# Performance work log

Measured on AMD Instinct MI355X. Metric: run time of the kernel, lower is better.

## Reference

```python
import math
import jax, jax.numpy as jnp
import numpy as np

B, S, D, H = 2, 2048, 2048, 16
HD = D // H  # head_dim = 128, rotary_dim = HD (full rotation)
ROPE_BASE = 10000.0


def setup_inputs() -> dict:
    key = jax.random.key(0)
    k0, k1, k2 = jax.random.split(key, 3)
    return {
        "x": jax.random.normal(k0, (B, S, D), dtype=jnp.float32),
        "Wqkv": jax.random.normal(k1, (D, 3 * D), dtype=jnp.float32) * 0.02,
        "bqkv": jnp.zeros((3 * D,), dtype=jnp.float32),
        "Wout": jax.random.normal(k2, (D, D), dtype=jnp.float32) * 0.02,
        "bout": jnp.zeros((D,), dtype=jnp.float32),
    }


def _rope_cos_sin(seqlen, dim):
    # flash-attn RotaryEmbedding: inv_freq over even indices, outer with positions
    inv_freq = 1.0 / (ROPE_BASE ** (jnp.arange(0, dim, 2, dtype=jnp.float32) / dim))
    t = jnp.arange(seqlen, dtype=jnp.float32)
    freqs = jnp.outer(t, inv_freq)  # (S, dim/2)
    return jnp.cos(freqs), jnp.sin(freqs)


def reference(x, Wqkv, bqkv, Wout, bout):
    b, s, d = x.shape
    hd = d // H
    # fused QKV projection -> (B, S, 3, H, HD)
    qkv = (x @ Wqkv + bqkv).reshape(b, s, 3, H, hd)
    q, k, v = qkv[:, :, 0], qkv[:, :, 1], qkv[:, :, 2]  # (B,S,H,HD)

    cos, sin = _rope_cos_sin(s, hd)
    c = cos[:, None, :]  # (S,1,HD/2) broadcast over heads
    si = sin[:, None, :]

    def rot(t):
        # split-half rotary (as in apply_rotary_emb_qkv), computed in fp32
        t1, t2 = jnp.split(t.astype(jnp.float32), 2, axis=-1)
        return jnp.concatenate([t1 * c - t2 * si, t1 * si + t2 * c], axis=-1).astype(x.dtype)

    q = rot(q)
    k = rot(k)

    scale = 1.0 / math.sqrt(hd)
    scores = jnp.einsum("bthd,bshd->bhts", q, k * scale)  # (B,H,S,S)
    causal_mask = jnp.triu(jnp.full((s, s), -10000.0, dtype=scores.dtype), 1)
    attn = jax.nn.softmax(scores + causal_mask, axis=-1)
    ctx = jnp.einsum("bhts,bshd->bthd", attn, v).reshape(b, s, d)
    return ctx @ Wout + bout
```

## Files before the change

### kernel.cpp

```cpp
#include <hip/hip_runtime.h>
#include <hip/hip_bf16.h>

typedef __attribute__((ext_vector_type(4))) float fx4;
typedef __attribute__((ext_vector_type(8))) short bx8;
typedef __hip_bfloat16 bf16;

#define GLD16(dst, src)                                                        \
  __builtin_amdgcn_global_load_lds(                                            \
      (__attribute__((address_space(1))) void*)(src),                          \
      (__attribute__((address_space(3))) void*)(dst), 16, 0, 0)

__device__ inline float bf2f(short s_) {
  unsigned int u = ((unsigned int)(unsigned short)s_) << 16;
  float f;
  __builtin_memcpy(&f, &u, 4);
  return f;
}
__device__ inline short f2bf(float f) {
  __hip_bfloat16 h = __float2bfloat16(f);
  short r;
  __builtin_memcpy(&r, &h, 2);
  return r;
}

__global__ __launch_bounds__(256) void k_cast(const float* __restrict__ in,
                                              bf16* __restrict__ out, int n4) {
  int i = blockIdx.x * 256 + threadIdx.x;
  if (i >= n4) return;
  float4 v = reinterpret_cast<const float4*>(in)[i];
  bf16 t[4] = {__float2bfloat16(v.x), __float2bfloat16(v.y),
               __float2bfloat16(v.z), __float2bfloat16(v.w)};
  reinterpret_cast<ushort4*>(out)[i] = *reinterpret_cast<ushort4*>(t);
}

__global__ void k_tcast(const float* __restrict__ in, bf16* __restrict__ out,
                        int R, int C) {
  __shared__ float tile[32][33];
  int c0 = blockIdx.x * 32, r0 = blockIdx.y * 32;
  int tx = threadIdx.x, ty = threadIdx.y;
#pragma unroll
  for (int j = 0; j < 4; ++j)
    tile[ty + j * 8][tx] = in[(size_t)(r0 + ty + j * 8) * C + c0 + tx];
  __syncthreads();
#pragma unroll
  for (int j = 0; j < 4; ++j)
    out[(size_t)(c0 + ty + j * 8) * R + r0 + tx] =
        __float2bfloat16(tile[tx][ty + j * 8]);
}

__global__ __launch_bounds__(256) void k_ropetab(float* __restrict__ cosT,
                                                 float* __restrict__ sinT) {
  int idx = blockIdx.x * 256 + threadIdx.x;
  int t = idx >> 6, i = idx & 63;
  float inv = expf(-logf(10000.0f) * (float)i * (1.0f / 64.0f));
  float fr = (float)t * inv;
  cosT[idx] = cosf(fr);
  sinT[idx] = sinf(fr);
}

__global__ __launch_bounds__(256) void k_rope(bf16* __restrict__ qkv,
                                              const float* __restrict__ cosT,
                                              const float* __restrict__ sinT) {
  int t = blockIdx.x * 256 + threadIdx.x;
  int d0 = (t & 7) * 8;
  int qk = (t >> 3) & 1;
  int h = (t >> 4) & 15;
  int s = (t >> 8) & 2047;
  int b = (t >> 19) & 1;
  bf16* base = qkv + (size_t)(b * 2048 + s) * 6144 + qk * 2048 + h * 128;
  bx8 lo = *(const bx8*)(base + d0);
  bx8 hi = *(const bx8*)(base + 64 + d0);
  float4 ca = *(const float4*)&cosT[s * 64 + d0];
  float4 cb = *(const float4*)&cosT[s * 64 + d0 + 4];
  float4 sa = *(const float4*)&sinT[s * 64 + d0];
  float4 sb = *(const float4*)&sinT[s * 64 + d0 + 4];
  float c[8] = {ca.x, ca.y, ca.z, ca.w, cb.x, cb.y, cb.z, cb.w};
  float si[8] = {sa.x, sa.y, sa.z, sa.w, sb.x, sb.y, sb.z, sb.w};
  bx8 olo, ohi;
#pragma unroll
  for (int e = 0; e < 8; ++e) {
    float t1 = bf2f(lo[e]), t2 = bf2f(hi[e]);
    olo[e] = f2bf(t1 * c[e] - t2 * si[e]);
    ohi[e] = f2bf(t1 * si[e] + t2 * c[e]);
  }
  *(bx8*)(base + d0) = olo;
  *(bx8*)(base + 64 + d0) = ohi;
}

__global__ void k_vtrans(const bf16* __restrict__ qkv, bf16* __restrict__ vT) {
  __shared__ bf16 tile[32][33];
  int s0 = blockIdx.x * 32, d0 = blockIdx.y * 32, bh = blockIdx.z;
  int b = bh >> 4, h = bh & 15;
  int tx = threadIdx.x, ty = threadIdx.y;
#pragma unroll
  for (int j = 0; j < 4; ++j)
    tile[ty + j * 8][tx] =
        qkv[(size_t)(b * 2048 + s0 + ty + j * 8) * 6144 + 4096 + h * 128 + d0 + tx];
  __syncthreads();
#pragma unroll
  for (int j = 0; j < 4; ++j)
    vT[(size_t)(bh * 128 + d0 + ty + j * 8) * 2048 + s0 + tx] = tile[tx][ty + j * 8];
}

__global__ __launch_bounds__(512, 2) void k_gemm256(
    const bf16* __restrict__ A, const bf16* __restrict__ BT,
    const float* __restrict__ bias, bf16* __restrict__ C, int M, int N, int K,
    int NBX) {
  __shared__ __align__(16) bf16 As[2][2][256 * 32];
  __shared__ __align__(16) bf16 Bs[2][2][256 * 32];
  const int tid = threadIdx.x;
  const int lane = tid & 63, wid = tid >> 6;
  const int lr = lane & 15, lg = lane >> 4;
  const int wr = wid >> 2, wc = wid & 3;
  const int nwg = gridDim.x, bid = blockIdx.x;
  const int swz = (bid & 7) * (nwg >> 3) + (bid >> 3);
  const int mb = swz / NBX, nb = swz - mb * NBX;
  const int m0 = mb * 256, n0 = nb * 256;
  const int NT = K >> 6;

  fx4 acc[8][4];
#pragma unroll
  for (int m = 0; m < 8; ++m)
#pragma unroll
    for (int n = 0; n < 4; ++n) acc[m][n] = (fx4)(0.0f);

  auto SA = [&](int buf, int ks, int t) {
#pragma unroll
    for (int q = 0; q < 2; ++q) {
      const int L = q * 512 + tid;
      const int row = L >> 2, u = L & 3;
      GLD16(&As[buf][ks][L * 8],
            A + (size_t)(m0 + row) * K + t * 64 + ks * 32 + ((u ^ (row & 3)) * 8));
    }
  };
  auto SB = [&](int buf, int ks, int t) {
#pragma unroll
    for (int q = 0; q < 2; ++q) {
      const int L = q * 512 + tid;
      const int row = L >> 2, u = L & 3;
      GLD16(&Bs[buf][ks][L * 8],
            BT + (size_t)(n0 + row) * K + t * 64 + ks * 32 + ((u ^ (row & 3)) * 8));
    }
  };

  bx8 af[4], bfr[4];
  auto LDA = [&](int buf, int ks, int mh) {
#pragma unroll
    for (int m = 0; m < 4; ++m) {
      const int r = wr * 128 + mh * 64 + m * 16 + lr;
      af[m] = *(const bx8*)&As[buf][ks][r * 32 + ((lg ^ (r & 3)) * 8)];
    }
  };
  auto LDB = [&](int buf, int ks) {
#pragma unroll
    for (int n = 0; n < 4; ++n) {
      const int r = wc * 64 + n * 16 + lr;
      bfr[n] = *(const bx8*)&Bs[buf][ks][r * 32 + ((lg ^ (r & 3)) * 8)];
    }
  };

#define MFMA16(MH)                                                             \
  asm volatile("s_waitcnt lgkmcnt(0)" ::: "memory");                           \
  __builtin_amdgcn_sched_barrier(0);                                           \
  __builtin_amdgcn_s_setprio(1);                                               \
  _Pragma("unroll") for (int m = 0; m < 4; ++m)                                \
      _Pragma("unroll") for (int n = 0; n < 4; ++n) acc[(MH)*4 + m][n] =       \
          __builtin_amdgcn_mfma_f32_16x16x32_bf16(af[m], bfr[n],               \
                                                  acc[(MH)*4 + m][n], 0, 0, 0);\
  __builtin_amdgcn_s_setprio(0);                                               \
  __builtin_amdgcn_s_barrier();

  SA(0, 0, 0); SB(0, 0, 0);
  SA(0, 1, 0); SB(0, 1, 0);
  SA(1, 0, 1); SB(1, 0, 1);
  asm volatile("s_waitcnt vmcnt(8)" ::: "memory");
  __builtin_amdgcn_s_barrier();

  for (int t = 0; t < NT; ++t) {
    const int buf = t & 1;
    LDA(buf, 0, 0); LDB(buf, 0);
    if (t + 1 < NT) SA(buf ^ 1, 1, t + 1);
    __builtin_amdgcn_s_barrier();
    MFMA16(0)
    LDA(buf, 0, 1);
    if (t + 1 < NT) SB(buf ^ 1, 1, t + 1);
    asm volatile("s_waitcnt vmcnt(8)" ::: "memory");
    __builtin_amdgcn_s_barrier();
    MFMA16(1)
    LDA(buf, 1, 0); LDB(buf, 1);
    if (t + 2 < NT) SA(buf, 0, t + 2);
    __builtin_amdgcn_s_barrier();
    MFMA16(0)
    LDA(buf, 1, 1);
    if (t + 2 < NT) SB(buf, 0, t + 2);
    asm volatile("s_waitcnt vmcnt(8)" ::: "memory");
    __builtin_amdgcn_s_barrier();
    MFMA16(1)
  }
#undef MFMA16

  float bv[4];
#pragma unroll
  for (int n = 0; n < 4; ++n) bv[n] = bias[n0 + wc * 64 + n * 16 + lr];
#pragma unroll
  for (int mm = 0; mm < 8; ++mm)
#pragma unroll
    for (int n = 0; n < 4; ++n) {
      const int col = n0 + wc * 64 + n * 16 + lr;
#pragma unroll
      for (int j = 0; j < 4; ++j) {
        const int row = m0 + wr * 128 + mm * 16 + lg * 4 + j;
        C[(size_t)row * N + col] = __float2bfloat16(acc[mm][n][j] + bv[n]);
      }
    }
}

__global__ __launch_bounds__(256) void k_gemm_bt(
    const bf16* __restrict__ A, const bf16* __restrict__ BT,
    const float* __restrict__ bias, void* __restrict__ Cp, int M, int N, int K,
    int out_bf16) {
  __shared__ __align__(16) bf16 As[128 * 64];
  __shared__ __align__(16) bf16 Bs[128 * 64];
  const int tid = threadIdx.x;
  const int m0 = blockIdx.y * 128, n0 = blockIdx.x * 128;
  const int lane = tid & 63, w = tid >> 6;
  const int lr = lane & 15, lg = lane >> 4;
  const int wr = w >> 1, wc = w & 1;

  fx4 acc[4][4];
#pragma unroll
  for (int m = 0; m < 4; ++m)
#pragma unroll
    for (int n = 0; n < 4; ++n) acc[m][n] = (fx4)(0.0f);

  for (int kt = 0; kt < K; kt += 64) {
#pragma unroll
    for (int q = 0; q < 4; ++q) {
      const int slot = q * 256 + tid;
      const int row = slot >> 3, u = slot & 7;
      const int us = (u ^ (row & 7)) * 8;
      GLD16(&As[slot * 8], A + (size_t)(m0 + row) * K + kt + us);
      GLD16(&Bs[slot * 8], BT + (size_t)(n0 + row) * K + kt + us);
    }
    __syncthreads();
#pragma unroll
    for (int ks = 0; ks < 2; ++ks) {
      bx8 af[4], bf[4];
#pragma unroll
      for (int m = 0; m < 4; ++m) {
        const int r = wr * 64 + m * 16 + lr;
        const int u = ((ks * 4 + lg) ^ (lr & 7)) * 8;
        af[m] = *(const bx8*)&As[r * 64 + u];
      }
#pragma unroll
      for (int n = 0; n < 4; ++n) {
        const int r = wc * 64 + n * 16 + lr;
        const int u = ((ks * 4 + lg) ^ (lr & 7)) * 8;
        bf[n] = *(const bx8*)&Bs[r * 64 + u];
      }
#pragma unroll
      for (int m = 0; m < 4; ++m)
#pragma unroll
        for (int n = 0; n < 4; ++n)
          acc[m][n] =
              __builtin_amdgcn_mfma_f32_16x16x32_bf16(af[m], bf[n], acc[m][n], 0, 0, 0);
    }
    __syncthreads();
  }

  float bv[4];
#pragma unroll
  for (int n = 0; n < 4; ++n) bv[n] = bias[n0 + wc * 64 + n * 16 + lr];

#pragma unroll
  for (int m = 0; m < 4; ++m)
#pragma unroll
    for (int n = 0; n < 4; ++n) {
      const int col = n0 + wc * 64 + n * 16 + lr;
#pragma unroll
      for (int j = 0; j < 4; ++j) {
        const int row = m0 + wr * 64 + m * 16 + lg * 4 + j;
        const float v = acc[m][n][j] + bv[n];
        if (out_bf16)
          ((bf16*)Cp)[(size_t)row * N + col] = __float2bfloat16(v);
        else
          ((float*)Cp)[(size_t)row * N + col] = v;
      }
    }
}

__global__ __launch_bounds__(256) void k_zero(float4* __restrict__ p) {
  p[blockIdx.x * 256 + threadIdx.x] = make_float4(0.f, 0.f, 0.f, 0.f);
}

#define ATT_SL2E 0.12751740f

__global__ __launch_bounds__(256, 2) void k_attn2(
    const bf16* __restrict__ qkv, const bf16* __restrict__ vT,
    bf16* __restrict__ ctx, float* __restrict__ Of32, float* __restrict__ lf32) {
  __shared__ __align__(16) bf16 Ks[2][128 * 128];
  __shared__ __align__(16) bf16 Ps[4][32 * 64];
  const int tid = threadIdx.x;
  const int lane = tid & 63, w = tid >> 6;
  const int lr = lane & 15, lg = lane >> 4;
  const int bid = blockIdx.x;
  const int u = bid >> 5, bh = bid & 31;
  const int b = bh >> 4, h = bh & 15;
  int qt, t0, t1;
  if (u < 8) {
    qt = 8 + u; t0 = 0; t1 = 8;
  } else if (u < 16) {
    qt = 23 - u; t0 = 8; t1 = qt + 1;
  } else {
    qt = 23 - u; t0 = 0; t1 = qt + 1;
  }
  const int single = (u >= 16);
  const int nt = t1 - t0;

  const bf16* kbase = qkv + (size_t)b * 2048 * 6144 + 2048 + h * 128;
  const bf16* vbase = vT + (size_t)(b * 16 + h) * 128 * 2048;

  auto STAGE = [&](int bufi, int kt) {
    const int kv0 = kt * 128;
#pragma unroll
    for (int q = 0; q < 8; ++q) {
      const int slot = q * 256 + tid;
      const int row = slot >> 4, uu = slot & 15;
      GLD16(&Ks[bufi][slot * 8],
            kbase + (size_t)(kv0 + row) * 6144 + ((uu ^ (row & 15)) * 8));
    }
  };

  const bf16* qbase =
      qkv + (size_t)(b * 2048 + qt * 128 + w * 32) * 6144 + h * 128;
  bx8 qf[2][4];
#pragma unroll
  for (int m = 0; m < 2; ++m)
#pragma unroll
    for (int ks = 0; ks < 4; ++ks)
      qf[m][ks] = *(const bx8*)(qbase + (size_t)(m * 16 + lr) * 6144 + ks * 32 + lg * 8);

  bx8 vones;
#pragma unroll
  for (int e = 0; e < 8; ++e) vones[e] = (short)0x3F80;

  fx4 oacc[2][8], lacc[2];
#pragma unroll
  for (int m = 0; m < 2; ++m) {
    lacc[m] = (fx4)(0.0f);
#pragma unroll
    for (int d = 0; d < 8; ++d) oacc[m][d] = (fx4)(0.0f);
  }

  const int qrow0 = qt * 128 + w * 32;

  STAGE(0, t0);
  for (int i = 0; i < nt; ++i) {
    const int kt = t0 + i;
    const int cur = i & 1;
    if (i + 1 < nt) {
      STAGE(cur ^ 1, kt + 1);
      asm volatile("s_waitcnt vmcnt(8)" ::: "memory");
    } else {
      asm volatile("s_waitcnt vmcnt(0)" ::: "memory");
    }
    __builtin_amdgcn_s_barrier();
    asm volatile("" ::: "memory");

#pragma unroll
    for (int h2 = 0; h2 < 2; ++h2) {
      const int kv0 = kt * 128 + h2 * 64;
      if (kv0 > qrow0 + 31) continue;

      fx4 sacc[2][4];
#pragma unroll
      for (int n = 0; n < 4; ++n) {
        sacc[0][n] = (fx4)(0.0f);
        sacc[1][n] = (fx4)(0.0f);
      }
      __builtin_amdgcn_s_setprio(1);
#pragma unroll
      for (int n = 0; n < 4; ++n) {
        const int r = h2 * 64 + n * 16 + lr;
#pragma unroll
        for (int ks = 0; ks < 4; ++ks) {
          const bx8 kf = *(const bx8*)&Ks[cur][r * 128 + (((ks * 4 + lg) ^ lr) * 8)];
          sacc[0][n] =
              __builtin_amdgcn_mfma_f32_16x16x32_bf16(qf[0][ks], kf, sacc[0][n], 0, 0, 0);
          sacc[1][n] =
              __builtin_amdgcn_mfma_f32_16x16x32_bf16(qf[1][ks], kf, sacc[1][n], 0, 0, 0);
        }
      }
      __builtin_amdgcn_s_setprio(0);

      const bool needmask = (kv0 + 63) > qrow0;
#pragma unroll
      for (int n = 0; n < 4; ++n) {
        const int kvi = kv0 + n * 16 + lr;
#pragma unroll
        for (int m = 0; m < 2; ++m)
#pragma unroll
          for (int j = 0; j < 4; ++j) {
            float v = sacc[m][n][j] * ATT_SL2E;
            if (needmask) {
              const int qi = qrow0 + m * 16 + lg * 4 + j;
              if (kvi > qi) v = -200.0f;
            }
            const float p = exp2f(fminf(v, 60.0f));
            const int r = m * 16 + lg * 4 + j, c = n * 16 + lr;
            const int c2 = (c & 7) | (((c >> 3) ^ (r & 7)) << 3);
            Ps[w][r * 64 + c2] = __float2bfloat16(p);
          }
      }

      __builtin_amdgcn_s_setprio(1);
#pragma unroll
      for (int ks2 = 0; ks2 < 2; ++ks2) {
        const int uu = ((ks2 * 4 + lg) ^ (lr & 7)) * 8;
        const bx8 pf0 = *(const bx8*)&Ps[w][(0 * 16 + lr) * 64 + uu];
        const bx8 pf1 = *(const bx8*)&Ps[w][(1 * 16 + lr) * 64 + uu];
        lacc[0] = __builtin_amdgcn_mfma_f32_16x16x32_bf16(pf0, vones, lacc[0], 0, 0, 0);
        lacc[1] = __builtin_amdgcn_mfma_f32_16x16x32_bf16(pf1, vones, lacc[1], 0, 0, 0);
#pragma unroll
        for (int dn = 0; dn < 8; ++dn) {
          const bx8 vf = *(const bx8*)(vbase + (size_t)(dn * 16 + lr) * 2048 + kv0 +
                                       ks2 * 32 + lg * 8);
          oacc[0][dn] =
              __builtin_amdgcn_mfma_f32_16x16x32_bf16(pf0, vf, oacc[0][dn], 0, 0, 0);
          oacc[1][dn] =
              __builtin_amdgcn_mfma_f32_16x16x32_bf16(pf1, vf, oacc[1][dn], 0, 0, 0);
        }
      }
      __builtin_amdgcn_s_setprio(0);
    }
    __builtin_amdgcn_s_barrier();
    asm volatile("" ::: "memory");
  }

  if (single) {
    float rl[2][4];
#pragma unroll
    for (int m = 0; m < 2; ++m)
#pragma unroll
      for (int j = 0; j < 4; ++j) rl[m][j] = 1.0f / lacc[m][j];
#pragma unroll
    for (int m = 0; m < 2; ++m)
#pragma unroll
      for (int dn = 0; dn < 8; ++dn)
#pragma unroll
        for (int j = 0; j < 4; ++j) {
          const int row = qt * 128 + w * 32 + m * 16 + lg * 4 + j;
          ctx[(size_t)(b * 2048 + row) * 2048 + h * 128 + dn * 16 + lr] =
              __float2bfloat16(oacc[m][dn][j] * rl[m][j]);
        }
  } else {
    float* obase =
        Of32 + (((size_t)(b * 16 + h)) * 1024 + (qt * 128 - 1024 + w * 32)) * 128;
#pragma unroll
    for (int m = 0; m < 2; ++m)
#pragma unroll
      for (int dn = 0; dn < 8; ++dn)
#pragma unroll
        for (int j = 0; j < 4; ++j)
          atomicAdd(&obase[(m * 16 + lg * 4 + j) * 128 + dn * 16 + lr],
                    oacc[m][dn][j]);
    if (lr == 0) {
      float* lbase =
          lf32 + ((size_t)(b * 16 + h)) * 1024 + (qt * 128 - 1024 + w * 32);
#pragma unroll
      for (int m = 0; m < 2; ++m)
#pragma unroll
        for (int j = 0; j < 4; ++j)
          atomicAdd(&lbase[m * 16 + lg * 4 + j], lacc[m][j]);
    }
  }
}

__global__ __launch_bounds__(256) void k_norm(const float* __restrict__ Of32,
                                              const float* __restrict__ lf32,
                                              bf16* __restrict__ ctx) {
  const int idx = blockIdx.x * 256 + threadIdx.x;
  const size_t base = (size_t)idx * 8;
  const int d = base & 127;
  const size_t rowi = base >> 7;
  const float rl = 1.0f / lf32[rowi];
  const float4 a = *(const float4*)&Of32[base];
  const float4 c = *(const float4*)&Of32[base + 4];
  const int s = (int)(rowi & 1023);
  const int bh = (int)(rowi >> 10);
  const int b = bh >> 4, h = bh & 15;
  bf16 o[8] = {__float2bfloat16(a.x * rl), __float2bfloat16(a.y * rl),
               __float2bfloat16(a.z * rl), __float2bfloat16(a.w * rl),
               __float2bfloat16(c.x * rl), __float2bfloat16(c.y * rl),
               __float2bfloat16(c.z * rl), __float2bfloat16(c.w * rl)};
  *(ushort4*)&ctx[(size_t)(b * 2048 + 1024 + s) * 2048 + h * 128 + d] =
      *(ushort4*)o;
  *(ushort4*)&ctx[(size_t)(b * 2048 + 1024 + s) * 2048 + h * 128 + d + 4] =
      *(ushort4*)(o + 4);
}

extern "C" void kernel_launch(void* const* d_in, const int* in_sizes, int n_in,
                              void* d_out, int out_size, void* d_ws, size_t ws_size,
                              hipStream_t stream) {
  const float* x = (const float*)d_in[0];
  const float* Wqkv = (const float*)d_in[1];
  const float* bqkv = (const float*)d_in[2];
  const float* Wout = (const float*)d_in[3];
  const float* bout = (const float*)d_in[4];
  float* out = (float*)d_out;

  char* ws = (char*)d_ws;
  bf16* xb    = (bf16*)(ws + 0);
  bf16* wqkvT = (bf16*)(ws + 16777216);
  bf16* woutT = (bf16*)(ws + 41943040);
  bf16* qkvb  = (bf16*)(ws + 50331648);
  bf16* vTb   = (bf16*)(ws + 100663296);
  bf16* ctxb  = (bf16*)(ws + 117440512);
  float* cosT = (float*)(ws + 134217728);
  float* sinT = (float*)(ws + 134742016);
  float* Of32 = (float*)(ws + 135266304);
  float* lf32 = (float*)(ws + 152043520);

  k_zero<<<4128, 256, 0, stream>>>((float4*)Of32);
  k_cast<<<8192, 256, 0, stream>>>(x, xb, 2097152);
  k_tcast<<<dim3(192, 64), dim3(32, 8), 0, stream>>>(Wqkv, wqkvT, 2048, 6144);
  k_tcast<<<dim3(64, 64), dim3(32, 8), 0, stream>>>(Wout, woutT, 2048, 2048);
  k_ropetab<<<512, 256, 0, stream>>>(cosT, sinT);
  k_gemm256<<<384, 512, 0, stream>>>(xb, wqkvT, bqkv, qkvb, 4096, 6144, 2048, 24);
  k_rope<<<4096, 256, 0, stream>>>(qkvb, cosT, sinT);
  k_vtrans<<<dim3(64, 4, 32), dim3(32, 8), 0, stream>>>(qkvb, vTb);
  k_attn2<<<768, 256, 0, stream>>>(qkvb, vTb, ctxb, Of32, lf32);
  k_norm<<<2048, 256, 0, stream>>>(Of32, lf32, ctxb);
  k_gemm_bt<<<dim3(16, 32), 256, 0, stream>>>(ctxb, woutT, bout, out, 4096, 2048,
                                              2048, 0);
}
```

Measured before the change: 345.6 us.

## Shrink QKV GEMM tile to 256x128 and replace split-K atomics with two partial buffers

The QKV projection GEMM moves from a 256x256 tile with a two-substep K=64 pipeline to a 256x128 tile with a simple double-buffered K=32 loop. This doubles the grid to 768 blocks and raises the occupancy hint, at the cost of less operand reuse and a full vmcnt(0) wait every iteration. Separately, the split attention tiles now write plain stores into two partial O/l buffers instead of atomically adding into one zeroed buffer. The combine kernel sums the two partials and normalises them, and the zeroing kernel is removed. The partial buffers reuse workspace that held the already-consumed bf16 x and Wqkv^T.

```diff
diff --git a/kernel.cpp b/kernel.cpp
--- a/kernel.cpp
+++ b/kernel.cpp
@@ -102,115 +102,88 @@
     vT[(size_t)(bh * 128 + d0 + ty + j * 8) * 2048 + s0 + tx] = tile[tx][ty + j * 8];
 }
 
-__global__ __launch_bounds__(512, 2) void k_gemm256(
+__global__ __launch_bounds__(512, 4) void k_gemm256(
     const bf16* __restrict__ A, const bf16* __restrict__ BT,
     const float* __restrict__ bias, bf16* __restrict__ C, int M, int N, int K,
     int NBX) {
-  __shared__ __align__(16) bf16 As[2][2][256 * 32];
-  __shared__ __align__(16) bf16 Bs[2][2][256 * 32];
+  __shared__ __align__(16) bf16 As[2][256 * 32];
+  __shared__ __align__(16) bf16 Bs[2][128 * 32];
   const int tid = threadIdx.x;
   const int lane = tid & 63, wid = tid >> 6;
   const int lr = lane & 15, lg = lane >> 4;
-  const int wr = wid >> 2, wc = wid & 3;
+  const int wr = wid >> 1, wc = wid & 1;
   const int nwg = gridDim.x, bid = blockIdx.x;
   const int swz = (bid & 7) * (nwg >> 3) + (bid >> 3);
   const int mb = swz / NBX, nb = swz - mb * NBX;
-  const int m0 = mb * 256, n0 = nb * 256;
-  const int NT = K >> 6;
-
-  fx4 acc[8][4];
-#pragma unroll
-  for (int m = 0; m < 8; ++m)
+  const int m0 = mb * 256, n0 = nb * 128;
+  const int NT = K >> 5;
+
+  fx4 acc[4][4];
+#pragma unroll
+  for (int m = 0; m < 4; ++m)
 #pragma unroll
     for (int n = 0; n < 4; ++n) acc[m][n] = (fx4)(0.0f);
 
-  auto SA = [&](int buf, int ks, int t) {
+  auto SA = [&](int buf, int t) {
 #pragma unroll
     for (int q = 0; q < 2; ++q) {
       const int L = q * 512 + tid;
       const int row = L >> 2, u = L & 3;
-      GLD16(&As[buf][ks][L * 8],
-            A + (size_t)(m0 + row) * K + t * 64 + ks * 32 + ((u ^ (row & 3)) * 8));
+      GLD16(&As[buf][L * 8],
+            A + (size_t)(m0 + row) * K + t * 32 + ((u ^ ((row >> 1) & 3)) * 8));
     }
   };
-  auto SB = [&](int buf, int ks, int t) {
-#pragma unroll
-    for (int q = 0; q < 2; ++q) {
-      const int L = q * 512 + tid;
-      const int row = L >> 2, u = L & 3;
-      GLD16(&Bs[buf][ks][L * 8],
-            BT + (size_t)(n0 + row) * K + t * 64 + ks * 32 + ((u ^ (row & 3)) * 8));
-    }
+  auto SB = [&](int buf, int t) {
+    const int L = tid;
+    const int row = L >> 2, u = L & 3;
+    GLD16(&Bs[buf][L * 8],
+          BT + (size_t)(n0 + row) * K + t * 32 + ((u ^ ((row >> 1) & 3)) * 8));
   };
 
-  bx8 af[4], bfr[4];
-  auto LDA = [&](int buf, int ks, int mh) {
+  SA(0, 0); SB(0, 0);
+  asm volatile("s_waitcnt vmcnt(0)" ::: "memory");
+  __builtin_amdgcn_s_barrier();
+
+  for (int t = 0; t < NT; ++t) {
+    const int buf = t & 1;
+    if (t + 1 < NT) { SA(buf ^ 1, t + 1); SB(buf ^ 1, t + 1); }
+    bx8 af[4], bfr[4];
 #pragma unroll
     for (int m = 0; m < 4; ++m) {
-      const int r = wr * 128 + mh * 64 + m * 16 + lr;
-      af[m] = *(const bx8*)&As[buf][ks][r * 32 + ((lg ^ (r & 3)) * 8)];
-    }
-  };
-  auto LDB = [&](int buf, int ks) {
+      const int r = wr * 64 + m * 16 + lr;
+      af[m] = *(const bx8*)&As[buf][r * 32 + ((lg ^ ((r >> 1) & 3)) * 8)];
+    }
 #pragma unroll
     for (int n = 0; n < 4; ++n) {
       const int r = wc * 64 + n * 16 + lr;
-      bfr[n] = *(const bx8*)&Bs[buf][ks][r * 32 + ((lg ^ (r & 3)) * 8)];
-    }
-  };
-
-#define MFMA16(MH)                                                             \
-  asm volatile("s_waitcnt lgkmcnt(0)" ::: "memory");                           \
-  __builtin_amdgcn_sched_barrier(0);                                           \
-  __builtin_amdgcn_s_setprio(1);                                               \
-  _Pragma("unroll") for (int m = 0; m < 4; ++m)                                \
-      _Pragma("unroll") for (int n = 0; n < 4; ++n) acc[(MH)*4 + m][n] =       \
-          __builtin_amdgcn_mfma_f32_16x16x32_bf16(af[m], bfr[n],               \
-                                                  acc[(MH)*4 + m][n], 0, 0, 0);\
-  __builtin_amdgcn_s_setprio(0);                                               \
-  __builtin_amdgcn_s_barrier();
-
-  SA(0, 0, 0); SB(0, 0, 0);
-  SA(0, 1, 0); SB(0, 1, 0);
-  SA(1, 0, 1); SB(1, 0, 1);
-  asm volatile("s_waitcnt vmcnt(8)" ::: "memory");
-  __builtin_amdgcn_s_barrier();
-
-  for (int t = 0; t < NT; ++t) {
-    const int buf = t & 1;
-    LDA(buf, 0, 0); LDB(buf, 0);
-    if (t + 1 < NT) SA(buf ^ 1, 1, t + 1);
+      bfr[n] = *(const bx8*)&Bs[buf][r * 32 + ((lg ^ ((r >> 1) & 3)) * 8)];
+    }
+    asm volatile("s_waitcnt lgkmcnt(0)" ::: "memory");
+    __builtin_amdgcn_sched_barrier(0);
+    __builtin_amdgcn_s_setprio(1);
+#pragma unroll
+    for (int m = 0; m < 4; ++m)
+#pragma unroll
+      for (int n = 0; n < 4; ++n)
+        acc[m][n] =
+            __builtin_amdgcn_mfma_f32_16x16x32_bf16(af[m], bfr[n], acc[m][n], 0, 0, 0);
+    __builtin_amdgcn_s_setprio(0);
+    asm volatile("s_waitcnt vmcnt(0)" ::: "memory");
     __builtin_amdgcn_s_barrier();
-    MFMA16(0)
-    LDA(buf, 0, 1);
-    if (t + 1 < NT) SB(buf ^ 1, 1, t + 1);
-    asm volatile("s_waitcnt vmcnt(8)" ::: "memory");
-    __builtin_amdgcn_s_barrier();
-    MFMA16(1)
-    LDA(buf, 1, 0); LDB(buf, 1);
-    if (t + 2 < NT) SA(buf, 0, t + 2);
-    __builtin_amdgcn_s_barrier();
-    MFMA16(0)
-    LDA(buf, 1, 1);
-    if (t + 2 < NT) SB(buf, 0, t + 2);
-    asm volatile("s_waitcnt vmcnt(8)" ::: "memory");
-    __builtin_amdgcn_s_barrier();
-    MFMA16(1)
-  }
-#undef MFMA16
+  }
 
   float bv[4];
 #pragma unroll
   for (int n = 0; n < 4; ++n) bv[n] = bias[n0 + wc * 64 + n * 16 + lr];
 #pragma unroll
-  for (int mm = 0; mm < 8; ++mm)
+  for (int m = 0; m < 4; ++m)
 #pragma unroll
     for (int n = 0; n < 4; ++n) {
       const int col = n0 + wc * 64 + n * 16 + lr;
 #pragma unroll
       for (int j = 0; j < 4; ++j) {
-        const int row = m0 + wr * 128 + mm * 16 + lg * 4 + j;
-        C[(size_t)row * N + col] = __float2bfloat16(acc[mm][n][j] + bv[n]);
+        const int row = m0 + wr * 64 + m * 16 + lg * 4 + j;
+        C[(size_t)row * N + col] = __float2bfloat16(acc[m][n][j] + bv[n]);
       }
     }
 }
@@ -289,15 +262,12 @@
     }
 }
 
-__global__ __launch_bounds__(256) void k_zero(float4* __restrict__ p) {
-  p[blockIdx.x * 256 + threadIdx.x] = make_float4(0.f, 0.f, 0.f, 0.f);
-}
-
 #define ATT_SL2E 0.12751740f
 
 __global__ __launch_bounds__(256, 2) void k_attn2(
     const bf16* __restrict__ qkv, const bf16* __restrict__ vT,
-    bf16* __restrict__ ctx, float* __restrict__ Of32, float* __restrict__ lf32) {
+    bf16* __restrict__ ctx, float* __restrict__ O0, float* __restrict__ O1,
+    float* __restrict__ l0, float* __restrict__ l1) {
   __shared__ __align__(16) bf16 Ks[2][128 * 128];
   __shared__ __align__(16) bf16 Ps[4][32 * 64];
   const int tid = threadIdx.x;
@@ -454,49 +424,52 @@
               __float2bfloat16(oacc[m][dn][j] * rl[m][j]);
         }
   } else {
+    float* Op = (u < 8) ? O0 : O1;
+    float* lp = (u < 8) ? l0 : l1;
     float* obase =
-        Of32 + (((size_t)(b * 16 + h)) * 1024 + (qt * 128 - 1024 + w * 32)) * 128;
+        Op + (((size_t)(b * 16 + h)) * 1024 + (qt * 128 - 1024 + w * 32)) * 128;
 #pragma unroll
     for (int m = 0; m < 2; ++m)
 #pragma unroll
       for (int dn = 0; dn < 8; ++dn)
 #pragma unroll
         for (int j = 0; j < 4; ++j)
-          atomicAdd(&obase[(m * 16 + lg * 4 + j) * 128 + dn * 16 + lr],
-                    oacc[m][dn][j]);
+          obase[(m * 16 + lg * 4 + j) * 128 + dn * 16 + lr] = oacc[m][dn][j];
     if (lr == 0) {
       float* lbase =
-          lf32 + ((size_t)(b * 16 + h)) * 1024 + (qt * 128 - 1024 + w * 32);
+          lp + ((size_t)(b * 16 + h)) * 1024 + (qt * 128 - 1024 + w * 32);
 #pragma unroll
       for (int m = 0; m < 2; ++m)
 #pragma unroll
-        for (int j = 0; j < 4; ++j)
-          atomicAdd(&lbase[m * 16 + lg * 4 + j], lacc[m][j]);
-    }
-  }
-}
-
-__global__ __launch_bounds__(256) void k_norm(const float* __restrict__ Of32,
-                                              const float* __restrict__ lf32,
+        for (int j = 0; j < 4; ++j) lbase[m * 16 + lg * 4 + j] = lacc[m][j];
+    }
+  }
+}
+
+__global__ __launch_bounds__(256) void k_comb(const float* __restrict__ O0,
+                                              const float* __restrict__ O1,
+                                              const float* __restrict__ l0,
+                                              const float* __restrict__ l1,
                                               bf16* __restrict__ ctx) {
   const int idx = blockIdx.x * 256 + threadIdx.x;
   const size_t base = (size_t)idx * 8;
-  const int d = base & 127;
   const size_t rowi = base >> 7;
-  const float rl = 1.0f / lf32[rowi];
-  const float4 a = *(const float4*)&Of32[base];
-  const float4 c = *(const float4*)&Of32[base + 4];
+  const float rl = 1.0f / (l0[rowi] + l1[rowi]);
+  const float4 a0 = *(const float4*)&O0[base];
+  const float4 b0 = *(const float4*)&O0[base + 4];
+  const float4 a1 = *(const float4*)&O1[base];
+  const float4 b1 = *(const float4*)&O1[base + 4];
+  const int d = (int)(base & 127);
   const int s = (int)(rowi & 1023);
   const int bh = (int)(rowi >> 10);
   const int b = bh >> 4, h = bh & 15;
-  bf16 o[8] = {__float2bfloat16(a.x * rl), __float2bfloat16(a.y * rl),
-               __float2bfloat16(a.z * rl), __float2bfloat16(a.w * rl),
-               __float2bfloat16(c.x * rl), __float2bfloat16(c.y * rl),
-               __float2bfloat16(c.z * rl), __float2bfloat16(c.w * rl)};
-  *(ushort4*)&ctx[(size_t)(b * 2048 + 1024 + s) * 2048 + h * 128 + d] =
-      *(ushort4*)o;
-  *(ushort4*)&ctx[(size_t)(b * 2048 + 1024 + s) * 2048 + h * 128 + d + 4] =
-      *(ushort4*)(o + 4);
+  bf16 o[8] = {__float2bfloat16((a0.x + a1.x) * rl), __float2bfloat16((a0.y + a1.y) * rl),
+               __float2bfloat16((a0.z + a1.z) * rl), __float2bfloat16((a0.w + a1.w) * rl),
+               __float2bfloat16((b0.x + b1.x) * rl), __float2bfloat16((b0.y + b1.y) * rl),
+               __float2bfloat16((b0.z + b1.z) * rl), __float2bfloat16((b0.w + b1.w) * rl)};
+  bf16* p = ctx + (size_t)(b * 2048 + 1024 + s) * 2048 + h * 128 + d;
+  *(ushort4*)p = *(ushort4*)o;
+  *(ushort4*)(p + 4) = *(ushort4*)(o + 4);
 }
 
 extern "C" void kernel_launch(void* const* d_in, const int* in_sizes, int n_in,
@@ -518,19 +491,20 @@
   bf16* ctxb  = (bf16*)(ws + 117440512);
   float* cosT = (float*)(ws + 134217728);
   float* sinT = (float*)(ws + 134742016);
-  float* Of32 = (float*)(ws + 135266304);
-  float* lf32 = (float*)(ws + 152043520);
-
-  k_zero<<<4128, 256, 0, stream>>>((float4*)Of32);
+  float* O0 = (float*)(ws + 0);
+  float* O1 = (float*)(ws + 16777216);
+  float* l0 = (float*)(ws + 33554432);
+  float* l1 = (float*)(ws + 33685504);
+
   k_cast<<<8192, 256, 0, stream>>>(x, xb, 2097152);
   k_tcast<<<dim3(192, 64), dim3(32, 8), 0, stream>>>(Wqkv, wqkvT, 2048, 6144);
   k_tcast<<<dim3(64, 64), dim3(32, 8), 0, stream>>>(Wout, woutT, 2048, 2048);
   k_ropetab<<<512, 256, 0, stream>>>(cosT, sinT);
-  k_gemm256<<<384, 512, 0, stream>>>(xb, wqkvT, bqkv, qkvb, 4096, 6144, 2048, 24);
+  k_gemm256<<<768, 512, 0, stream>>>(xb, wqkvT, bqkv, qkvb, 4096, 6144, 2048, 48);
   k_rope<<<4096, 256, 0, stream>>>(qkvb, cosT, sinT);
   k_vtrans<<<dim3(64, 4, 32), dim3(32, 8), 0, stream>>>(qkvb, vTb);
-  k_attn2<<<768, 256, 0, stream>>>(qkvb, vTb, ctxb, Of32, lf32);
-  k_norm<<<2048, 256, 0, stream>>>(Of32, lf32, ctxb);
+  k_attn2<<<768, 256, 0, stream>>>(qkvb, vTb, ctxb, O0, O1, l0, l1);
+  k_comb<<<2048, 256, 0, stream>>>(O0, O1, l0, l1, ctxb);
   k_gemm_bt<<<dim3(16, 32), 256, 0, stream>>>(ctxb, woutT, bout, out, 4096, 2048,
                                               2048, 0);
 }
```

Result: faster. 336.7 us (-2.6%).
